# Performance work log

Measured on AMD Instinct MI355X. Metric: run time of the kernel, lower is better.

Reference implementation:

```python
import jax, jax.numpy as jnp
import numpy as np

B, S, D, H, L = 2, 2048, 768, 12, 12
DH = D // H
REL_POS_BINS, MAX_REL_POS = 32, 128
REL_2D_POS_BINS, MAX_REL_2D_POS = 64, 256
LN_EPS = 1e-12


def setup_inputs() -> dict:
    key = jax.random.key(0)
    ks = jax.random.split(key, 12)
    s = 0.02
    return {
        "hidden_states": jax.random.normal(ks[0], (B, S, D), jnp.float32),
        "attention_mask": jnp.zeros((B, 1, 1, S), jnp.bool_),  # True = masked
        "position_ids": jnp.sort(jax.random.randint(ks[1], (B, S), 0, 1024), axis=-1),
        "bbox": jax.random.randint(ks[2], (B, S, 4), 0, 1024),
        # stacked per-layer params (torch Linear applied as x @ W + b)
        "q_w": jax.random.normal(ks[3], (L, D, D), jnp.float32) * s,
        "q_b": jnp.zeros((L, D), jnp.float32),
        "k_w": jax.random.normal(ks[4], (L, D, D), jnp.float32) * s,
        "k_b": jnp.zeros((L, D), jnp.float32),
        "v_w": jax.random.normal(ks[5], (L, D, D), jnp.float32) * s,
        "v_b": jnp.zeros((L, D), jnp.float32),
        "o_w": jax.random.normal(ks[6], (L, D, D), jnp.float32) * s,
        "o_b": jnp.zeros((L, D), jnp.float32),
        "ln_g": jnp.ones((L, D), jnp.float32),
        "ln_b": jnp.zeros((L, D), jnp.float32),
        # rel-pos bias heads x buckets (nn.Linear(bins, heads, bias=False).weight)
        "rel_pos_bias_w": jax.random.normal(ks[7], (H, REL_POS_BINS), jnp.float32) * s,
        "rel_x_bias_w": jax.random.normal(ks[8], (H, REL_2D_POS_BINS), jnp.float32) * s,
        "rel_y_bias_w": jax.random.normal(ks[9], (H, REL_2D_POS_BINS), jnp.float32) * s,
    }


def _rel_bucket(rel, num_buckets, max_distance):
    # bidirectional bucketing from Mesh-TF / ErnieLayout
    nb = num_buckets // 2
    ret = (rel > 0).astype(jnp.int32) * nb
    n = jnp.abs(rel).astype(jnp.int32)
    max_exact = nb // 2
    is_small = n < max_exact
    nf = jnp.maximum(n, 1).astype(jnp.float32)  # avoid log(0); masked by is_small
    val_large = max_exact + (
        jnp.log(nf / max_exact) / np.log(max_distance / max_exact) * (nb - max_exact)
    ).astype(jnp.int32)
    val_large = jnp.minimum(val_large, nb - 1)
    return ret + jnp.where(is_small, n, val_large)


def _bias_from_table(ids_1d, table, num_buckets, max_distance):
    # ids_1d: [B,S] int; table: [H, buckets] -> bias [B,H,S,S]
    rel = ids_1d[:, None, :] - ids_1d[:, :, None]  # memory - query
    buckets = _rel_bucket(rel, num_buckets, max_distance)  # [B,S,S]
    return jnp.transpose(table.T[buckets], (0, 3, 1, 2))  # one-hot @ W.T == gather


def _layer_norm(x, g, b):
    m = jnp.mean(x, axis=-1, keepdims=True)
    v = jnp.mean((x - m) ** 2, axis=-1, keepdims=True)
    return (x - m) / jnp.sqrt(v + LN_EPS) * g + b


def reference(hidden_states, attention_mask, position_ids, bbox,
              q_w, q_b, k_w, k_b, v_w, v_b, o_w, o_b, ln_g, ln_b,
              rel_pos_bias_w, rel_x_bias_w, rel_y_bias_w):
    rel_pos = _bias_from_table(position_ids, rel_pos_bias_w, REL_POS_BINS, MAX_REL_POS)
    rel_2d = (_bias_from_table(bbox[:, :, 0], rel_x_bias_w, REL_2D_POS_BINS, MAX_REL_2D_POS)
              + _bias_from_table(bbox[:, :, 3], rel_y_bias_w, REL_2D_POS_BINS, MAX_REL_2D_POS))
    bias = rel_pos + rel_2d  # [B,H,S,S], shared across layers
    neg = jnp.finfo(jnp.float32).min
    inv_sqrt_dh = 1.0 / np.sqrt(DH)

    def layer(h, p):
        qw, qb, kw, kb, vw, vb, ow, ob, g, bb = p
        q = (h @ qw + qb).reshape(B, S, H, DH).transpose(0, 2, 1, 3) * inv_sqrt_dh
        k = (h @ kw + kb).reshape(B, S, H, DH).transpose(0, 2, 1, 3)
        v = (h @ vw + vb).reshape(B, S, H, DH).transpose(0, 2, 1, 3)
        scores = jnp.einsum('bhqd,bhkd->bhqk', q, k) + bias
        scores = jnp.where(attention_mask, neg, scores)
        probs = jax.nn.softmax(scores, axis=-1)
        ctx = jnp.einsum('bhqk,bhkd->bhqd', probs, v).transpose(0, 2, 1, 3).reshape(B, S, D)
        out = ctx @ ow + ob  # ErnieLayoutSelfOutput dense
        return _layer_norm(out + h, g, bb), None

    h, _ = jax.lax.scan(layer, hidden_states,
                        (q_w, q_b, k_w, k_b, v_w, v_b, o_w, o_b, ln_g, ln_b))
    return h
```

## Files before the change

### kernel.cpp

```cpp
#include <hip/hip_runtime.h>


#define BB 2
#define SS 2048
#define DD 768
#define HH 12
#define NLAYER 12
#define MM 4096

typedef unsigned short u16;
typedef unsigned char u8;
typedef __attribute__((ext_vector_type(8))) short bf16x8;
typedef __attribute__((ext_vector_type(4))) float f32x4;
typedef __attribute__((ext_vector_type(2))) float f32x2;

#define LOG2E 1.44269504088896340736f

__device__ __forceinline__ u16 f2bf(float f) {
  unsigned u = __float_as_uint(f);
  unsigned r = (u + 0x7FFFu + ((u >> 16) & 1u)) >> 16;
  return (u16)r;
}
__device__ __forceinline__ unsigned cvtpk(float a, float b) {
  unsigned r;
  asm("v_cvt_pk_bf16_f32 %0, %1, %2" : "=v"(r) : "v"(a), "v"(b));
  return r;
}
__device__ __forceinline__ float exp2v(float x) {
  float r;
  asm("v_exp_f32 %0, %1" : "=v"(r) : "v"(x));
  return r;
}

__device__ __forceinline__ void g2lds16(const void* g, void* l) {
  __builtin_amdgcn_global_load_lds(
      (const __attribute__((address_space(1))) unsigned int*)g,
      (__attribute__((address_space(3))) unsigned int*)l, 16, 0, 0);
}

__global__ __launch_bounds__(256) void k_hb(const float4* __restrict__ x,
                                            uint2* __restrict__ o, int n4) {
  int i = blockIdx.x * 256 + threadIdx.x;
  if (i < n4) {
    float4 v = x[i];
    uint2 r;
    r.x = (unsigned)f2bf(v.x) | ((unsigned)f2bf(v.y) << 16);
    r.y = (unsigned)f2bf(v.z) | ((unsigned)f2bf(v.w) << 16);
    o[i] = r;
  }
}

__device__ __forceinline__ int bucket1(int rel) {
  int ret = rel > 0 ? 16 : 0;
  int n = rel < 0 ? -rel : rel;
  if (n < 8) return ret + n;
  int v = 8 + (int)(logf((float)n * 0.125f) * 2.8853900817779268f);
  return ret + (v < 15 ? v : 15);
}
__device__ __forceinline__ int bucket2(int rel) {
  int ret = rel > 0 ? 32 : 0;
  int n = rel < 0 ? -rel : rel;
  if (n < 16) return ret + n;
  int v = 16 + (int)(logf((float)n * 0.0625f) * 5.7707801635558537f);
  return ret + (v < 31 ? v : 31);
}

__global__ __launch_bounds__(256) void k_bias(
    const int* __restrict__ pos, const int* __restrict__ bbx,
    const unsigned char* __restrict__ msk,
    const float* __restrict__ wp, const float* __restrict__ wx,
    const float* __restrict__ wy, u8* __restrict__ bias) {
  int bid = blockIdx.x;
  int b = bid >> 10, qt = (bid >> 5) & 31, kt = bid & 31;
  __shared__ __align__(16) float swpT[3][32][4], swxT[3][64][4], swyT[3][64][4];
  __shared__ int pq[64], xq[64], yq[64], pk[64], xk[64], yk[64];
  __shared__ unsigned char mk[64];
  int t = threadIdx.x;
  for (int i = t; i < 384; i += 256) {
    int g = i >> 7, idx = i & 127;
    swpT[g][idx >> 2][idx & 3] = wp[(g * 4 + (idx & 3)) * 32 + (idx >> 2)] * LOG2E;
  }
  for (int i = t; i < 768; i += 256) {
    int g = i >> 8, idx = i & 255;
    swxT[g][idx >> 2][idx & 3] = wx[(g * 4 + (idx & 3)) * 64 + (idx >> 2)] * LOG2E;
    swyT[g][idx >> 2][idx & 3] = wy[(g * 4 + (idx & 3)) * 64 + (idx >> 2)] * LOG2E;
  }
  int q0 = qt * 64, k0 = kt * 64;
  if (t < 64) {
    int gi = b * SS + q0 + t;
    pq[t] = pos[gi]; xq[t] = bbx[gi * 4]; yq[t] = bbx[gi * 4 + 3];
  } else if (t < 128) {
    int j = t - 64, gi = b * SS + k0 + j;
    pk[j] = pos[gi]; xk[j] = bbx[gi * 4]; yk[j] = bbx[gi * 4 + 3];
    mk[j] = msk[b * SS + k0 + j];
  }
  __syncthreads();
  int w = t >> 6, l = t & 63;
  int hi = l >> 4;
  int qlr = w * 16 + (l & 15);
  int pql = pq[qlr], xql = xq[qlr], yql = yq[qlr];
  int packed[16];
#pragma unroll
  for (int fn = 0; fn < 4; fn++)
#pragma unroll
    for (int r = 0; r < 4; r++) {
      int kl = fn * 16 + hi * 4 + r;
      int b1 = bucket1(pk[kl] - pql);
      int b2 = bucket2(xk[kl] - xql);
      int b3 = bucket2(yk[kl] - yql);
      packed[fn * 4 + r] = b1 | (b2 << 5) | (b3 << 11) | (mk[kl] ? (1 << 17) : 0);
    }
  for (int hg = 0; hg < 3; hg++) {
    unsigned words[4][4];
#pragma unroll
    for (int j2 = 0; j2 < 8; j2++) {
      float a0[4], a1[4];
      {
        int p = packed[2 * j2];
        f32x4 ap = *(const f32x4*)swpT[hg][p & 31];
        f32x4 bx = *(const f32x4*)swxT[hg][(p >> 5) & 63];
        f32x4 cy = *(const f32x4*)swyT[hg][(p >> 11) & 63];
        bool mm = (p >> 17) != 0;
#pragma unroll
        for (int hh = 0; hh < 4; hh++)
          a0[hh] = mm ? -3.0e38f : (ap[hh] + bx[hh] + cy[hh]);
      }
      {
        int p = packed[2 * j2 + 1];
        f32x4 ap = *(const f32x4*)swpT[hg][p & 31];
        f32x4 bx = *(const f32x4*)swxT[hg][(p >> 5) & 63];
        f32x4 cy = *(const f32x4*)swyT[hg][(p >> 11) & 63];
        bool mm = (p >> 17) != 0;
#pragma unroll
        for (int hh = 0; hh < 4; hh++)
          a1[hh] = mm ? -3.0e38f : (ap[hh] + bx[hh] + cy[hh]);
      }
      int wd = j2 >> 1;
      if ((j2 & 1) == 0) {
#pragma unroll
        for (int hh = 0; hh < 4; hh++)
          words[hh][wd] = __builtin_amdgcn_cvt_pk_fp8_f32(a0[hh], a1[hh], 0, false);
      } else {
#pragma unroll
        for (int hh = 0; hh < 4; hh++)
          words[hh][wd] = __builtin_amdgcn_cvt_pk_fp8_f32(a0[hh], a1[hh],
                                                          words[hh][wd], true);
      }
    }
#pragma unroll
    for (int hh = 0; hh < 4; hh++) {
      int h = hg * 4 + hh;
      u8* dst = bias +
          ((size_t)((b * 12 + h) * 1024 + qt * 32 + kt) * 256 + t) * 16;
      *(uint4*)dst = make_uint4(words[hh][0], words[hh][1], words[hh][2],
                                words[hh][3]);
    }
  }
}

__global__ __launch_bounds__(256) void k_wconv(
    const float* __restrict__ qw, const float* __restrict__ kw,
    const float* __restrict__ vw, const float* __restrict__ ow, int layer,
    u16* __restrict__ wt) {
  int bid = blockIdx.x;
  int g = bid / 144, rr_ = bid % 144, nt = rr_ / 12, kt = rr_ % 12;
  const float* src = g == 0 ? qw : g == 1 ? kw : g == 2 ? vw : ow;
  src += (size_t)layer * DD * DD;
  __shared__ float sm[64][67];
  int t = threadIdx.x, c2 = t & 31, r0 = t >> 5;
#pragma unroll
  for (int p = 0; p < 8; p++) {
    int row = r0 + p * 8;
    float2 v = *(const float2*)&src[(size_t)(kt * 64 + row) * DD + nt * 64 + c2 * 2];
    sm[row][c2 * 2] = v.x;
    sm[row][c2 * 2 + 1] = v.y;
  }
  __syncthreads();
  u16* dst = wt + (size_t)g * DD * DD;
#pragma unroll
  for (int p = 0; p < 8; p++) {
    int n = r0 + p * 8;
    float v0 = sm[c2 * 2][n], v1 = sm[c2 * 2 + 1][n];
    *(unsigned*)&dst[(size_t)(nt * 64 + n) * DD + kt * 64 + c2 * 2] = cvtpk(v0, v1);
  }
}

__device__ __forceinline__ void gemm_core(const u16* __restrict__ A,
                                          const u16* __restrict__ Bt, u16* As,
                                          u16* Bs, f32x4 acc[4][4], int tid) {
  int w = tid >> 6, l = tid & 63;
  int wm = w >> 1, wn = w & 1;
#pragma unroll
  for (int i = 0; i < 4; i++)
#pragma unroll
    for (int j = 0; j < 4; j++) acc[i][j] = f32x4{0.f, 0.f, 0.f, 0.f};
  for (int kt = 0; kt < 12; kt++) {
    __syncthreads();
    int r0 = w * 32;
#pragma unroll
    for (int j = 0; j < 4; j++) {
      int row = r0 + j * 8 + (l >> 3);
      int sl = (l & 7) ^ (row & 7);
      g2lds16(A + (size_t)row * DD + kt * 64 + sl * 8, As + (r0 + j * 8) * 64);
      g2lds16(Bt + (size_t)row * DD + kt * 64 + sl * 8, Bs + (r0 + j * 8) * 64);
    }
    __syncthreads();
#pragma unroll
    for (int kk = 0; kk < 2; kk++) {
      bf16x8 af[4], bfr[4];
#pragma unroll
      for (int fm = 0; fm < 4; fm++) {
        int row = wm * 64 + fm * 16 + (l & 15);
        int slot = (kk * 4 + (l >> 4)) ^ (row & 7);
        af[fm] = *(const bf16x8*)((const char*)As + row * 128 + slot * 16);
      }
#pragma unroll
      for (int fn = 0; fn < 4; fn++) {
        int row = wn * 64 + fn * 16 + (l & 15);
        int slot = (kk * 4 + (l >> 4)) ^ (row & 7);
        bfr[fn] = *(const bf16x8*)((const char*)Bs + row * 128 + slot * 16);
      }
#pragma unroll
      for (int fm = 0; fm < 4; fm++)
#pragma unroll
        for (int fn = 0; fn < 4; fn++)
          acc[fm][fn] = __builtin_amdgcn_mfma_f32_16x16x32_bf16(
              af[fm], bfr[fn], acc[fm][fn], 0, 0, 0);
    }
  }
}

__global__ __launch_bounds__(256) void k_gemm_qkv(
    const u16* __restrict__ hb, const u16* __restrict__ wt,
    const float* __restrict__ qbias, const float* __restrict__ kbias,
    const float* __restrict__ vbias, u16* __restrict__ qo, u16* __restrict__ ko,
    u16* __restrict__ vo) {
  __shared__ __align__(16) u16 As[128 * 64];
  __shared__ __align__(16) u16 Bs[128 * 64];
  int bid = blockIdx.x;
  int mblk = bid / 18, nblk = bid % 18;
  int g = nblk / 6, nb = nblk % 6;
  const u16* A = hb + (size_t)mblk * 128 * DD;
  const u16* Bt = wt + (size_t)g * DD * DD + (size_t)nb * 128 * DD;
  f32x4 acc[4][4];
  gemm_core(A, Bt, As, Bs, acc, threadIdx.x);
  const float* bias = g == 0 ? qbias : g == 1 ? kbias : vbias;
  u16* out = g == 0 ? qo : g == 1 ? ko : vo;
  float scale = g == 0 ? 0.125f * LOG2E : 1.0f;
  int w = threadIdx.x >> 6, l = threadIdx.x & 63;
  int wm = w >> 1, wn = w & 1;
#pragma unroll
  for (int fn = 0; fn < 4; fn++) {
    int col = nb * 128 + wn * 64 + fn * 16 + (l & 15);
    float bval = bias[col];
#pragma unroll
    for (int fm = 0; fm < 4; fm++)
#pragma unroll
      for (int r = 0; r < 4; r++) {
        int row = mblk * 128 + wm * 64 + fm * 16 + ((l >> 4) << 2) + r;
        out[(size_t)row * DD + col] = f2bf((acc[fm][fn][r] + bval) * scale);
      }
  }
}

__global__ __launch_bounds__(256) void k_gemm_o(const u16* __restrict__ ctx,
                                                const u16* __restrict__ wto,
                                                const float* __restrict__ obias,
                                                float* __restrict__ outp) {
  __shared__ __align__(16) u16 As[128 * 64];
  __shared__ __align__(16) u16 Bs[128 * 64];
  int bid = blockIdx.x;
  int mblk = bid / 6, nblk = bid % 6;
  const u16* A = ctx + (size_t)mblk * 128 * DD;
  const u16* Bt = wto + (size_t)nblk * 128 * DD;
  f32x4 acc[4][4];
  gemm_core(A, Bt, As, Bs, acc, threadIdx.x);
  int w = threadIdx.x >> 6, l = threadIdx.x & 63;
  int wm = w >> 1, wn = w & 1;
#pragma unroll
  for (int fn = 0; fn < 4; fn++) {
    int col = nblk * 128 + wn * 64 + fn * 16 + (l & 15);
    float bval = obias[col];
#pragma unroll
    for (int fm = 0; fm < 4; fm++)
#pragma unroll
      for (int r = 0; r < 4; r++) {
        int row = mblk * 128 + wm * 64 + fm * 16 + ((l >> 4) << 2) + r;
        outp[(size_t)row * DD + col] = acc[fm][fn][r] + bval;
      }
  }
}

__global__ __launch_bounds__(256) void k_vt(const u16* __restrict__ vo,
                                            u16* __restrict__ vt) {
  int bid = blockIdx.x;
  int bh = bid >> 5, st = bid & 31;
  int b = bh / 12, h = bh % 12;
  int s0 = st * 64;
  __shared__ u16 sm[64][68];
  int t = threadIdx.x, c = t & 63, r0 = t >> 6;
#pragma unroll
  for (int p = 0; p < 16; p++) {
    int r = r0 + p * 4;
    sm[r][c] = vo[(size_t)(b * SS + s0 + r) * DD + h * 64 + c];
  }
  __syncthreads();
#pragma unroll
  for (int p = 0; p < 16; p++) {
    int d = r0 + p * 4;
    vt[(size_t)(bh * 64 + d) * SS + s0 + c] = sm[c][d];
  }
}

__global__ __launch_bounds__(256) void k_attn(
    const u16* __restrict__ qm, const u16* __restrict__ kmat,
    const u16* __restrict__ vt, const u8* __restrict__ bias,
    u16* __restrict__ ctx) {
  int bid = blockIdx.x;
  int qt = bid & 31, bh = bid >> 5;
  int b = bh / 12, h = bh % 12;
  __shared__ __align__(16) u16 Ks[2][64 * 64];
  __shared__ __align__(16) u16 Vs[2][64 * 64];
  __shared__ __align__(16) u16 Ps[4][16 * 64];
  int tid = threadIdx.x, w = tid >> 6, l = tid & 63;
  int hi = l >> 4, qr = l & 15;
  int q0 = qt * 64;
  const u16* qp = qm + (size_t)(b * SS + q0 + w * 16 + qr) * DD + h * 64 +
                  hi * 8;
  bf16x8 aq0 = *(const bf16x8*)qp;
  bf16x8 aq1 = *(const bf16x8*)(qp + 32);
  const u16* kb_ = kmat + (size_t)(b * SS) * DD + h * 64;
  const u16* vb_ = vt + (size_t)bh * 64 * SS;
  const u8* bb_ = bias + ((size_t)(bh * 32 + qt) * 32 * 256 + tid) * 16;
  f32x4 oa[4];
#pragma unroll
  for (int fn = 0; fn < 4; fn++) oa[fn] = f32x4{0.f, 0.f, 0.f, 0.f};
  f32x4 lacc = f32x4{0.f, 0.f, 0.f, 0.f};
  float m_ = -3.0e38f;
  bf16x8 vones;
#pragma unroll
  for (int i = 0; i < 8; i++) vones[i] = (short)0x3F80;
  int srow = tid >> 3, sc8 = tid & 7;

  auto STAGE = [&](int kt, int buf) {
#pragma unroll
    for (int j = 0; j < 2; j++) {
      int rr = srow + j * 32;
      int sl = sc8 ^ (rr & 7);
      g2lds16(kb_ + (size_t)(kt * 64 + rr) * DD + sl * 8,
              &Ks[buf][tid * 8 + j * 2048]);
      g2lds16(vb_ + (size_t)rr * SS + kt * 64 + sl * 8,
              &Vs[buf][tid * 8 + j * 2048]);
    }
  };

  STAGE(0, 0);
  uint4 bu = *(const uint4*)bb_;
  uint4 nb = bu;
  char* pw = (char*)&Ps[w][0] + qr * 128;
  int qs = (qr & 7) << 4;
  __syncthreads();

  for (int kt = 0; kt < 32; kt++) {
    int buf = kt & 1;
    if (kt < 31) {
      STAGE(kt + 1, buf ^ 1);
      nb = *(const uint4*)(bb_ + (size_t)(kt + 1) * 4096);
    }
    f32x4 sc[4];
    {
      unsigned uw[4] = {bu.x, bu.y, bu.z, bu.w};
#pragma unroll
      for (int fn = 0; fn < 4; fn++) {
        f32x2 p0 = __builtin_amdgcn_cvt_pk_f32_fp8(uw[fn], false);
        f32x2 p1 = __builtin_amdgcn_cvt_pk_f32_fp8(uw[fn], true);
        sc[fn][0] = p0.x; sc[fn][1] = p0.y; sc[fn][2] = p1.x; sc[fn][3] = p1.y;
      }
    }
    __builtin_amdgcn_s_setprio(1);
#pragma unroll
    for (int kk = 0; kk < 2; kk++) {
      bf16x8 aq = kk == 0 ? aq0 : aq1;
#pragma unroll
      for (int fn = 0; fn < 4; fn++) {
        int row = fn * 16 + qr;
        int slot = (kk * 4 + hi) ^ (row & 7);
        bf16x8 bk = *(const bf16x8*)((const char*)&Ks[buf][0] + row * 128 +
                                     slot * 16);
        sc[fn] = __builtin_amdgcn_mfma_f32_16x16x32_bf16(bk, aq, sc[fn],
                                                         0, 0, 0);
      }
    }
    __builtin_amdgcn_s_setprio(0);
    float pm = fmaxf(fmaxf(fmaxf(sc[0][0], sc[0][1]), fmaxf(sc[0][2], sc[0][3])),
                     fmaxf(fmaxf(sc[1][0], sc[1][1]), fmaxf(sc[1][2], sc[1][3])));
    pm = fmaxf(pm,
         fmaxf(fmaxf(fmaxf(sc[2][0], sc[2][1]), fmaxf(sc[2][2], sc[2][3])),
               fmaxf(fmaxf(sc[3][0], sc[3][1]), fmaxf(sc[3][2], sc[3][3]))));
    pm = fmaxf(pm, __shfl_xor(pm, 16));
    pm = fmaxf(pm, __shfl_xor(pm, 32));
    if (__any(pm > m_ + 8.f)) {
      float mn = fmaxf(m_, pm);
      float f = exp2v(m_ - mn);
#pragma unroll
      for (int fn = 0; fn < 4; fn++)
#pragma unroll
        for (int r = 0; r < 4; r++) oa[fn][r] *= f;
#pragma unroll
      for (int r = 0; r < 4; r++) lacc[r] *= f;
      m_ = mn;
    }
#pragma unroll
    for (int fn = 0; fn < 4; fn++)
#pragma unroll
      for (int r = 0; r < 4; r++) sc[fn][r] = exp2v(sc[fn][r] - m_);
#pragma unroll
    for (int fn = 0; fn < 4; fn++) {
      unsigned w0 = cvtpk(sc[fn][0], sc[fn][1]);
      unsigned w1 = cvtpk(sc[fn][2], sc[fn][3]);
      *(uint2*)(pw + ((fn * 32 + hi * 8) ^ qs)) = make_uint2(w0, w1);
    }
    __builtin_amdgcn_s_setprio(1);
#pragma unroll
    for (int ck = 0; ck < 2; ck++) {
      bf16x8 pt = *(const bf16x8*)(pw + ((ck * 64 + hi * 16) ^ qs));
#pragma unroll
      for (int fn = 0; fn < 4; fn++) {
        int row = fn * 16 + qr;
        int slot = (ck * 4 + hi) ^ (row & 7);
        bf16x8 av = *(const bf16x8*)((const char*)&Vs[buf][0] + row * 128 +
                                     slot * 16);
        oa[fn] = __builtin_amdgcn_mfma_f32_16x16x32_bf16(av, pt, oa[fn],
                                                         0, 0, 0);
      }
      lacc = __builtin_amdgcn_mfma_f32_16x16x32_bf16(vones, pt, lacc, 0, 0, 0);
    }
    __builtin_amdgcn_s_setprio(0);
    bu = nb;
    __syncthreads();
  }
  float inv = 1.0f / lacc[0];
  u16* cp = ctx + (size_t)(b * SS + q0 + w * 16 + qr) * DD + h * 64 + hi * 4;
#pragma unroll
  for (int fn = 0; fn < 4; fn++) {
    unsigned w0 = cvtpk(oa[fn][0] * inv, oa[fn][1] * inv);
    unsigned w1 = cvtpk(oa[fn][2] * inv, oa[fn][3] * inv);
    *(uint2*)(cp + fn * 16) = make_uint2(w0, w1);
  }
}

__global__ __launch_bounds__(256) void k_ln(const float* __restrict__ x,
                                            const float* __restrict__ res,
                                            const float* __restrict__ g,
                                            const float* __restrict__ bta,
                                            float* __restrict__ ho,
                                            u16* __restrict__ hbo) {
  int w = threadIdx.x >> 6, l = threadIdx.x & 63;
  int row = blockIdx.x * 4 + w;
  const float* xr = x + (size_t)row * DD;
  const float* rr = res + (size_t)row * DD;
  float v[12];
  float s = 0.f, s2 = 0.f;
#pragma unroll
  for (int j = 0; j < 12; j++) {
    float a = xr[l + j * 64] + rr[l + j * 64];
    v[j] = a;
    s += a;
    s2 += a * a;
  }
#pragma unroll
  for (int m = 1; m < 64; m <<= 1) {
    s += __shfl_xor(s, m);
    s2 += __shfl_xor(s2, m);
  }
  float mean = s * (1.f / 768.f);
  float var = s2 * (1.f / 768.f) - mean * mean;
  float rstd = rsqrtf(var + 1e-12f);
#pragma unroll
  for (int j = 0; j < 12; j++) {
    int c = l + j * 64;
    float y = (v[j] - mean) * rstd * g[c] + bta[c];
    ho[(size_t)row * DD + c] = y;
    hbo[(size_t)row * DD + c] = f2bf(y);
  }
}

extern "C" void kernel_launch(void* const* d_in, const int* in_sizes, int n_in,
                              void* d_out, int out_size, void* d_ws,
                              size_t ws_size, hipStream_t stream) {
  const float* hid = (const float*)d_in[0];
  const unsigned char* msk = (const unsigned char*)d_in[1];
  const int* pos = (const int*)d_in[2];
  const int* bbx = (const int*)d_in[3];
  const float* qw = (const float*)d_in[4];
  const float* qbv = (const float*)d_in[5];
  const float* kw = (const float*)d_in[6];
  const float* kbv = (const float*)d_in[7];
  const float* vw = (const float*)d_in[8];
  const float* vbv = (const float*)d_in[9];
  const float* ow = (const float*)d_in[10];
  const float* obv = (const float*)d_in[11];
  const float* lng = (const float*)d_in[12];
  const float* lnb = (const float*)d_in[13];
  const float* wpb = (const float*)d_in[14];
  const float* wxb = (const float*)d_in[15];
  const float* wyb = (const float*)d_in[16];
  float* outp = (float*)d_out;

  char* p = (char*)d_ws;
  u8* bias = (u8*)p;     p += (size_t)100663296;
  float* hbuf = (float*)p; p += 12582912;
  u16* hb = (u16*)p;     p += 6291456;
  u16* qo = (u16*)p;     p += 6291456;
  u16* ko = (u16*)p;     p += 6291456;
  u16* vo = (u16*)p;     p += 6291456;
  u16* vtb = (u16*)p;    p += 6291456;
  u16* ctxb = (u16*)p;   p += 6291456;
  u16* wtb = (u16*)p;    p += 4718592;
  float* att = (float*)qo;

  k_hb<<<dim3(3072), dim3(256), 0, stream>>>((const float4*)hid, (uint2*)hb,
                                             786432);
  k_bias<<<dim3(2048), dim3(256), 0, stream>>>(pos, bbx, msk, wpb, wxb, wyb,
                                               bias);
  for (int l = 0; l < NLAYER; l++) {
    k_wconv<<<dim3(576), dim3(256), 0, stream>>>(qw, kw, vw, ow, l, wtb);
    k_gemm_qkv<<<dim3(576), dim3(256), 0, stream>>>(
        hb, wtb, qbv + l * DD, kbv + l * DD, vbv + l * DD, qo, ko, vo);
    k_vt<<<dim3(768), dim3(256), 0, stream>>>(vo, vtb);
    k_attn<<<dim3(768), dim3(256), 0, stream>>>(qo, ko, vtb, bias, ctxb);
    k_gemm_o<<<dim3(192), dim3(256), 0, stream>>>(
        ctxb, wtb + (size_t)3 * DD * DD, obv + l * DD, att);
    k_ln<<<dim3(1024), dim3(256), 0, stream>>>(
        att, l == 0 ? hid : (const float*)hbuf, lng + l * DD, lnb + l * DD,
        l == 11 ? outp : hbuf, hb);
  }
}
```

Before: 1.532 ms.

## Fuse V transpose into QKV GEMM, batch weight conversion, swizzle block order

The QKV GEMM epilogue now writes V directly in transposed per-head layout, which removes the separate k_vt kernel and its extra round trip through global memory. All layers' weights are converted to bf16 in one launch before the loop instead of one conversion launch per layer, at the cost of a much larger weight workspace. Block indices in the GEMM and attention kernels are remapped with an interleave across groups of eight, likely to change how work spreads over XCDs and caches. The attention row max now uses v_max3 instructions. The transposed V stores are 8-byte scattered writes with a large stride, which may coalesce poorly.

Measured after the change: 1.429 ms. -6.7%, faster.

```diff
diff --git a/kernel.cpp b/kernel.cpp
--- a/kernel.cpp
+++ b/kernel.cpp
@@ -15,6 +15,7 @@
 typedef __attribute__((ext_vector_type(2))) float f32x2;
 
 #define LOG2E 1.44269504088896340736f
+#define WT_LSTRIDE 2359296
 
 __device__ __forceinline__ u16 f2bf(float f) {
   unsigned u = __float_as_uint(f);
@@ -29,6 +30,11 @@
 __device__ __forceinline__ float exp2v(float x) {
   float r;
   asm("v_exp_f32 %0, %1" : "=v"(r) : "v"(x));
+  return r;
+}
+__device__ __forceinline__ float max3f(float a, float b, float c) {
+  float r;
+  asm("v_max3_f32 %0, %1, %2, %3" : "=v"(r) : "v"(a), "v"(b), "v"(c));
   return r;
 }
 
@@ -158,12 +164,13 @@
   }
 }
 
-__global__ __launch_bounds__(256) void k_wconv(
+__global__ __launch_bounds__(256) void k_wconv_all(
     const float* __restrict__ qw, const float* __restrict__ kw,
-    const float* __restrict__ vw, const float* __restrict__ ow, int layer,
+    const float* __restrict__ vw, const float* __restrict__ ow,
     u16* __restrict__ wt) {
   int bid = blockIdx.x;
-  int g = bid / 144, rr_ = bid % 144, nt = rr_ / 12, kt = rr_ % 12;
+  int layer = bid / 576, rem = bid % 576;
+  int g = rem / 144, rr_ = rem % 144, nt = rr_ / 12, kt = rr_ % 12;
   const float* src = g == 0 ? qw : g == 1 ? kw : g == 2 ? vw : ow;
   src += (size_t)layer * DD * DD;
   __shared__ float sm[64][67];
@@ -176,7 +183,7 @@
     sm[row][c2 * 2 + 1] = v.y;
   }
   __syncthreads();
-  u16* dst = wt + (size_t)g * DD * DD;
+  u16* dst = wt + (size_t)layer * WT_LSTRIDE + (size_t)g * DD * DD;
 #pragma unroll
   for (int p = 0; p < 8; p++) {
     int n = r0 + p * 8;
@@ -234,21 +241,41 @@
     const u16* __restrict__ hb, const u16* __restrict__ wt,
     const float* __restrict__ qbias, const float* __restrict__ kbias,
     const float* __restrict__ vbias, u16* __restrict__ qo, u16* __restrict__ ko,
-    u16* __restrict__ vo) {
+    u16* __restrict__ vtb) {
   __shared__ __align__(16) u16 As[128 * 64];
   __shared__ __align__(16) u16 Bs[128 * 64];
-  int bid = blockIdx.x;
+  int bid0 = blockIdx.x;
+  int bid = (bid0 & 7) * 72 + (bid0 >> 3);
   int mblk = bid / 18, nblk = bid % 18;
   int g = nblk / 6, nb = nblk % 6;
   const u16* A = hb + (size_t)mblk * 128 * DD;
   const u16* Bt = wt + (size_t)g * DD * DD + (size_t)nb * 128 * DD;
   f32x4 acc[4][4];
   gemm_core(A, Bt, As, Bs, acc, threadIdx.x);
-  const float* bias = g == 0 ? qbias : g == 1 ? kbias : vbias;
-  u16* out = g == 0 ? qo : g == 1 ? ko : vo;
-  float scale = g == 0 ? 0.125f * LOG2E : 1.0f;
   int w = threadIdx.x >> 6, l = threadIdx.x & 63;
   int wm = w >> 1, wn = w & 1;
+  int hi4 = (l >> 4) << 2;
+  if (g == 2) {
+#pragma unroll
+    for (int fn = 0; fn < 4; fn++) {
+      int col = nb * 128 + wn * 64 + fn * 16 + (l & 15);
+      float bval = vbias[col];
+      int h = col >> 6, d = col & 63;
+#pragma unroll
+      for (int fm = 0; fm < 4; fm++) {
+        int row = mblk * 128 + wm * 64 + fm * 16 + hi4;
+        int bb = row >> 11, s = row & 2047;
+        unsigned p0 = cvtpk(acc[fm][fn][0] + bval, acc[fm][fn][1] + bval);
+        unsigned p1 = cvtpk(acc[fm][fn][2] + bval, acc[fm][fn][3] + bval);
+        *(uint2*)(vtb + ((size_t)(bb * 12 + h) * 64 + d) * 2048 + s) =
+            make_uint2(p0, p1);
+      }
+    }
+    return;
+  }
+  const float* bias = g == 0 ? qbias : kbias;
+  u16* out = g == 0 ? qo : ko;
+  float scale = g == 0 ? 0.125f * LOG2E : 1.0f;
 #pragma unroll
   for (int fn = 0; fn < 4; fn++) {
     int col = nb * 128 + wn * 64 + fn * 16 + (l & 15);
@@ -257,7 +284,7 @@
     for (int fm = 0; fm < 4; fm++)
 #pragma unroll
       for (int r = 0; r < 4; r++) {
-        int row = mblk * 128 + wm * 64 + fm * 16 + ((l >> 4) << 2) + r;
+        int row = mblk * 128 + wm * 64 + fm * 16 + hi4 + r;
         out[(size_t)row * DD + col] = f2bf((acc[fm][fn][r] + bval) * scale);
       }
   }
@@ -269,7 +296,8 @@
                                                 float* __restrict__ outp) {
   __shared__ __align__(16) u16 As[128 * 64];
   __shared__ __align__(16) u16 Bs[128 * 64];
-  int bid = blockIdx.x;
+  int bid0 = blockIdx.x;
+  int bid = (bid0 & 7) * 24 + (bid0 >> 3);
   int mblk = bid / 6, nblk = bid % 6;
   const u16* A = ctx + (size_t)mblk * 128 * DD;
   const u16* Bt = wto + (size_t)nblk * 128 * DD;
@@ -291,32 +319,12 @@
   }
 }
 
-__global__ __launch_bounds__(256) void k_vt(const u16* __restrict__ vo,
-                                            u16* __restrict__ vt) {
-  int bid = blockIdx.x;
-  int bh = bid >> 5, st = bid & 31;
-  int b = bh / 12, h = bh % 12;
-  int s0 = st * 64;
-  __shared__ u16 sm[64][68];
-  int t = threadIdx.x, c = t & 63, r0 = t >> 6;
-#pragma unroll
-  for (int p = 0; p < 16; p++) {
-    int r = r0 + p * 4;
-    sm[r][c] = vo[(size_t)(b * SS + s0 + r) * DD + h * 64 + c];
-  }
-  __syncthreads();
-#pragma unroll
-  for (int p = 0; p < 16; p++) {
-    int d = r0 + p * 4;
-    vt[(size_t)(bh * 64 + d) * SS + s0 + c] = sm[c][d];
-  }
-}
-
 __global__ __launch_bounds__(256) void k_attn(
     const u16* __restrict__ qm, const u16* __restrict__ kmat,
     const u16* __restrict__ vt, const u8* __restrict__ bias,
     u16* __restrict__ ctx) {
-  int bid = blockIdx.x;
+  int bid0 = blockIdx.x;
+  int bid = (bid0 & 7) * 96 + (bid0 >> 3);
   int qt = bid & 31, bh = bid >> 5;
   int b = bh / 12, h = bh % 12;
   __shared__ __align__(16) u16 Ks[2][64 * 64];
@@ -392,11 +400,14 @@
       }
     }
     __builtin_amdgcn_s_setprio(0);
-    float pm = fmaxf(fmaxf(fmaxf(sc[0][0], sc[0][1]), fmaxf(sc[0][2], sc[0][3])),
-                     fmaxf(fmaxf(sc[1][0], sc[1][1]), fmaxf(sc[1][2], sc[1][3])));
-    pm = fmaxf(pm,
-         fmaxf(fmaxf(fmaxf(sc[2][0], sc[2][1]), fmaxf(sc[2][2], sc[2][3])),
-               fmaxf(fmaxf(sc[3][0], sc[3][1]), fmaxf(sc[3][2], sc[3][3]))));
+    float pa = max3f(sc[0][0], sc[0][1], sc[0][2]);
+    float pb = max3f(sc[0][3], sc[1][0], sc[1][1]);
+    pa = max3f(pa, sc[1][2], sc[1][3]);
+    pb = max3f(pb, sc[2][0], sc[2][1]);
+    pa = max3f(pa, sc[2][2], sc[2][3]);
+    pb = max3f(pb, sc[3][0], sc[3][1]);
+    pa = max3f(pa, sc[3][2], sc[3][3]);
+    float pm = fmaxf(pa, pb);
     pm = fmaxf(pm, __shfl_xor(pm, 16));
     pm = fmaxf(pm, __shfl_xor(pm, 32));
     if (__any(pm > m_ + 8.f)) {
@@ -513,24 +524,23 @@
   u16* hb = (u16*)p;     p += 6291456;
   u16* qo = (u16*)p;     p += 6291456;
   u16* ko = (u16*)p;     p += 6291456;
-  u16* vo = (u16*)p;     p += 6291456;
   u16* vtb = (u16*)p;    p += 6291456;
   u16* ctxb = (u16*)p;   p += 6291456;
-  u16* wtb = (u16*)p;    p += 4718592;
+  u16* wtb = (u16*)p;    p += (size_t)56623104;
   float* att = (float*)qo;
 
   k_hb<<<dim3(3072), dim3(256), 0, stream>>>((const float4*)hid, (uint2*)hb,
                                              786432);
   k_bias<<<dim3(2048), dim3(256), 0, stream>>>(pos, bbx, msk, wpb, wxb, wyb,
                                                bias);
+  k_wconv_all<<<dim3(6912), dim3(256), 0, stream>>>(qw, kw, vw, ow, wtb);
   for (int l = 0; l < NLAYER; l++) {
-    k_wconv<<<dim3(576), dim3(256), 0, stream>>>(qw, kw, vw, ow, l, wtb);
+    const u16* wl = wtb + (size_t)l * WT_LSTRIDE;
     k_gemm_qkv<<<dim3(576), dim3(256), 0, stream>>>(
-        hb, wtb, qbv + l * DD, kbv + l * DD, vbv + l * DD, qo, ko, vo);
-    k_vt<<<dim3(768), dim3(256), 0, stream>>>(vo, vtb);
+        hb, wl, qbv + l * DD, kbv + l * DD, vbv + l * DD, qo, ko, vtb);
     k_attn<<<dim3(768), dim3(256), 0, stream>>>(qo, ko, vtb, bias, ctxb);
     k_gemm_o<<<dim3(192), dim3(256), 0, stream>>>(
-        ctxb, wtb + (size_t)3 * DD * DD, obv + l * DD, att);
+        ctxb, wl + (size_t)3 * DD * DD, obv + l * DD, att);
     k_ln<<<dim3(1024), dim3(256), 0, stream>>>(
         att, l == 0 ? hid : (const float*)hbuf, lng + l * DD, lnb + l * DD,
         l == 11 ? outp : hbuf, hb);
```
